# Kernel tuning notes

Hardware: AMD Instinct MI355X
Metric: run time of the kernel (lower is better)

The kernel has to match this reference:

```python
import jax, jax.numpy as jnp
import numpy as np

H = 12        # num_attention_heads
A = 16        # agent_num
C = 768       # hidden_size


def setup_inputs() -> dict:
    key = jax.random.key(0)
    ks = jax.random.split(key, 16)
    B, N = 8, 4096
    std = 0.02
    return {
        "s1_hidden_states": jax.random.normal(ks[0], (B, N, C), jnp.float32),
        "s2_hidden_states": jax.random.normal(ks[1], (B, N, C), jnp.float32),
        "Wq": jax.random.normal(ks[2], (C, C), jnp.float32) * std,
        "bq": jnp.zeros((C,), jnp.float32),
        "Wk": jax.random.normal(ks[3], (C, C), jnp.float32) * std,
        "bk": jnp.zeros((C,), jnp.float32),
        "Wv": jax.random.normal(ks[4], (C, C), jnp.float32) * std,
        "bv": jnp.zeros((C,), jnp.float32),
        "an_bias": jax.random.normal(ks[5], (H, A, 7, 7), jnp.float32) * std,
        "na_bias": jax.random.normal(ks[6], (H, A, 7, 7), jnp.float32) * std,
        "ah_bias": jax.random.normal(ks[7], (1, H, A, A, 1), jnp.float32) * std,
        "aw_bias": jax.random.normal(ks[8], (1, H, A, 1, A), jnp.float32) * std,
        "ha_bias": jax.random.normal(ks[9], (1, H, A, 1, A), jnp.float32) * std,
        "wa_bias": jax.random.normal(ks[10], (1, H, 1, A, A), jnp.float32) * std,
    }


def reference(s1_hidden_states, s2_hidden_states, Wq, bq, Wk, bk, Wv, bv,
              an_bias, na_bias, ah_bias, aw_bias, ha_bias, wa_bias):
    b, n, c = s1_hidden_states.shape
    m = s2_hidden_states.shape[1]
    hd = c // H
    scale = hd ** -0.5

    q = s1_hidden_states @ Wq.T + bq            # (b, n, c)
    k = s2_hidden_states @ Wk.T + bk            # (b, m, c)
    v = s2_hidden_states @ Wv.T + bv            # (b, m, c)

    # AdaptiveAvgPool1d(A) with n % A == 0 -> uniform chunk mean
    agent = q.reshape(b, A, n // A, c).mean(axis=2)  # (b, A, c)

    def heads(x):
        return x.reshape(b, -1, H, hd).transpose(0, 2, 1, 3)

    qh, kh, vh = heads(q), heads(k), heads(v)        # (b,H,·,hd)
    ah = heads(agent)                                # (b,H,A,hd)

    # stage 1: agent -> keys.  bias is constant per (h, a) row.
    pb1 = jax.image.resize(an_bias, (H, A, A, A), method='bilinear').reshape(1, H, A, A * A)
    pb2 = (ah_bias + aw_bias).reshape(1, H, A, A * A)
    pb = (pb1 + pb2).mean(axis=-1)                   # (1, H, A)
    agent_attn = jnp.einsum('bhad,bhmd->bham', ah * scale, kh) + pb[:, :, :, None]
    agent_attn = jax.nn.softmax(agent_attn, axis=-1)
    agent_v = jnp.einsum('bham,bhmd->bhad', agent_attn, vh)  # (b,H,A,hd)

    # stage 2: queries -> agents.
    ab1 = jax.image.resize(na_bias, (H, A, A, A), method='bilinear') \
            .reshape(1, H, A, A * A).transpose(0, 1, 3, 2)   # (1,H,A*A,A)
    ab2 = (ha_bias + wa_bias).reshape(1, H, A * A, A)
    ab = (ab1 + ab2).mean(axis=-2)                   # (1, H, A)
    q_attn = jnp.einsum('bhnd,bhad->bhna', qh * scale, ah) + ab[:, :, None, :]
    q_attn = jax.nn.softmax(q_attn, axis=-1)
    x = jnp.einsum('bhna,bhad->bhnd', q_attn, agent_v)  # (b,H,n,hd)
    return x.transpose(0, 2, 1, 3).reshape(b, n, c)
```

## Files before the change

### kernel.cpp

```cpp
#include <hip/hip_runtime.h>
#include <cstdint>
#include <cstddef>

typedef unsigned short ushort_t;
typedef unsigned int uint;

typedef __attribute__((ext_vector_type(8))) short short8;
typedef __attribute__((ext_vector_type(4))) float floatx4;

#define CDIM 768

__device__ __forceinline__ float bfu(ushort_t u) {
    return __uint_as_float(((uint)u) << 16);
}
__device__ __forceinline__ void bf2(uint u, float& lo, float& hi) {
    lo = __uint_as_float(u << 16);
    hi = __uint_as_float(u & 0xffff0000u);
}
__device__ __forceinline__ ushort_t f2bfu(float f) {
    uint u = __float_as_uint(f);
    u += 0x7fffu + ((u >> 16) & 1u);
    return (ushort_t)(u >> 16);
}
__device__ __forceinline__ uint pack2(float a, float b) {
    return (uint)f2bfu(a) | ((uint)f2bfu(b) << 16);
}
__device__ __forceinline__ uint cvt2(float lo, float hi) {
    uint r;
    asm("v_cvt_pk_bf16_f32 %0, %1, %2" : "=v"(r) : "v"(lo), "v"(hi));
    return r;
}
__device__ __forceinline__ short8 mk8(uint a, uint b, uint c, uint d) {
    union { uint4 u; short8 s; } x;
    x.u = (uint4){a, b, c, d};
    return x.s;
}
__device__ __forceinline__ void gload_lds16(const void* g, void* l) {
    __builtin_amdgcn_global_load_lds(
        (__attribute__((address_space(1))) void*)(uintptr_t)g,
        (__attribute__((address_space(3))) void*)l, 16, 0, 0);
}

__global__ __launch_bounds__(256) void cvt_w(
    const float* __restrict__ Wq, const float* __restrict__ Wk,
    const float* __restrict__ Wv, ushort_t* __restrict__ wb)
{
    const int m = blockIdx.y;
    const float* src = (m == 0) ? Wq : (m == 1 ? Wk : Wv);
    ushort_t* dst = wb + (size_t)m * 589824;
    const int i = (blockIdx.x * 256 + threadIdx.x) * 8;
    const float4 f0 = *(const float4*)(src + i);
    const float4 f1 = *(const float4*)(src + i + 4);
    uint4 u;
    u.x = pack2(f0.x, f0.y);
    u.y = pack2(f0.z, f0.w);
    u.z = pack2(f1.x, f1.y);
    u.w = pack2(f1.z, f1.w);
    *(uint4*)(dst + i) = u;
}

__global__ __launch_bounds__(256) void init_agent(const float* __restrict__ bq,
                                                  float* __restrict__ agent)
{
    const int bh = blockIdx.x;
    const int h = bh % 12;
    for (int i = threadIdx.x; i < 1024; i += 256)
        agent[(size_t)bh * 1024 + i] = bq[h * 64 + (i & 63)];
}

__global__ __launch_bounds__(256, 2) void gemm_qkv(
    const float* __restrict__ s1, const float* __restrict__ s2,
    const ushort_t* __restrict__ wb,
    const float* __restrict__ bq, const float* __restrict__ bk, const float* __restrict__ bv,
    ushort_t* __restrict__ qo, ushort_t* __restrict__ ko, ushort_t* __restrict__ vo,
    float* __restrict__ agent)
{
    const int z = blockIdx.z;
    const float* A        = (z == 0) ? s1 : s2;
    const ushort_t* W     = wb + (size_t)z * 589824;
    const float* bias     = (z == 0) ? bq : (z == 1 ? bk : bv);
    ushort_t* out         = (z == 0) ? qo : (z == 1 ? ko : vo);

    __shared__ ushort_t At[128 * 64];
    __shared__ ushort_t Wt[128 * 64];

    const int tid  = threadIdx.x;
    const int wave = tid >> 6;
    const int lane = tid & 63;
    const int wm = wave >> 1, wn = wave & 1;

    const int id   = blockIdx.x + (blockIdx.y << 8);
    const int id2  = (id & 7) * 192 + (id >> 3);
    const int row0 = (id2 / 6) * 128;
    const int col0 = (id2 % 6) * 128;

    const int sro = lane >> 3;
    const int sch = ((lane & 7) ^ sro) * 8;
    const float*    gaF = A + (size_t)(row0 + wave * 32 + sro) * CDIM + sch;
    const ushort_t* gwB = W + (size_t)(col0 + wave * 32 + sro) * CDIM + sch;

    floatx4 acc[4][4];
    #pragma unroll
    for (int i = 0; i < 4; ++i)
        #pragma unroll
        for (int j = 0; j < 4; ++j)
            acc[i][j] = (floatx4){0.f, 0.f, 0.f, 0.f};

    const int q4 = lane >> 4, r16 = lane & 15;

    float4 ra[4][2];
    #pragma unroll
    for (int i = 0; i < 4; ++i) {
        const float* p = gaF + (size_t)i * 8 * CDIM;
        ra[i][0] = *(const float4*)(p);
        ra[i][1] = *(const float4*)(p + 4);
    }

    for (int kt = 0; kt < CDIM; kt += 64) {
        __syncthreads();
        #pragma unroll
        for (int i = 0; i < 4; ++i)
            gload_lds16(gwB + (size_t)i * 8 * CDIM + kt, &Wt[(wave * 32 + i * 8) * 64]);
        #pragma unroll
        for (int i = 0; i < 4; ++i) {
            uint4 u;
            u.x = cvt2(ra[i][0].x, ra[i][0].y);
            u.y = cvt2(ra[i][0].z, ra[i][0].w);
            u.z = cvt2(ra[i][1].x, ra[i][1].y);
            u.w = cvt2(ra[i][1].z, ra[i][1].w);
            *(uint4*)&At[(wave * 32 + i * 8 + sro) * 64 + (lane & 7) * 8] = u;
        }
        __syncthreads();
        if (kt + 64 < CDIM) {
            #pragma unroll
            for (int i = 0; i < 4; ++i) {
                const float* p = gaF + (size_t)i * 8 * CDIM + kt + 64;
                ra[i][0] = *(const float4*)(p);
                ra[i][1] = *(const float4*)(p + 4);
            }
        }
        #pragma unroll
        for (int ks = 0; ks < 2; ++ks) {
            short8 af[4], bfr[4];
            #pragma unroll
            for (int mt = 0; mt < 4; ++mt) {
                const int row = wm * 64 + mt * 16 + r16;
                const int ch  = (ks * 4 + q4) ^ (row & 7);
                af[mt] = *(const short8*)&At[row * 64 + ch * 8];
            }
            #pragma unroll
            for (int nt = 0; nt < 4; ++nt) {
                const int row = wn * 64 + nt * 16 + r16;
                const int ch  = (ks * 4 + q4) ^ (row & 7);
                bfr[nt] = *(const short8*)&Wt[row * 64 + ch * 8];
            }
            #pragma unroll
            for (int mt = 0; mt < 4; ++mt)
                #pragma unroll
                for (int nt = 0; nt < 4; ++nt)
                    acc[mt][nt] = __builtin_amdgcn_mfma_f32_16x16x32_bf16(
                        af[mt], bfr[nt], acc[mt][nt], 0, 0, 0);
        }
    }

    const int b = row0 >> 12;
    const int m_base = row0 & 4095;
    #pragma unroll
    for (int nt = 0; nt < 4; ++nt) {
        const int col = col0 + wn * 64 + nt * 16 + r16;
        const int h = col >> 6, d = col & 63;
        const float bb = bias[col];
        ushort_t* ob = out + ((size_t)(b * 12 + h) * 4096) * 64 + d;
        float psum = 0.f;
        #pragma unroll
        for (int mt = 0; mt < 4; ++mt) {
            const int m = m_base + wm * 64 + mt * 16 + q4 * 4;
            #pragma unroll
            for (int r = 0; r < 4; ++r) {
                ob[(size_t)(m + r) * 64] = f2bfu(acc[mt][nt][r] + bb);
                psum += acc[mt][nt][r];
            }
        }
        if (z == 0) {
            psum += __shfl_xor(psum, 16);
            psum += __shfl_xor(psum, 32);
            if (q4 == 0)
                atomicAdd(&agent[(size_t)(b * 12 + h) * 1024 + (m_base >> 8) * 64 + d],
                          psum * (1.0f / 256.0f));
        }
    }
}

__global__ void bias_ab_k(const float* __restrict__ na, const float* __restrict__ ha,
                          const float* __restrict__ wa, float* __restrict__ ab)
{
    const int t = threadIdx.x;
    if (t >= 192) return;
    const int h = t >> 4, a = t & 15;
    const float cw[7] = {2.25f, 2.34375f, 2.28125f, 2.25f, 2.28125f, 2.34375f, 2.25f};
    float acc = 0.f;
    const float* nb = na + (h * 16 + a) * 49;
    for (int i = 0; i < 7; ++i)
        for (int j = 0; j < 7; ++j)
            acc += cw[i] * cw[j] * nb[i * 7 + j];
    acc *= (1.0f / 256.0f);
    float s = 0.f;
    for (int p = 0; p < 16; ++p)
        s += ha[(h * 16 + p) * 16 + a] + wa[(h * 16 + p) * 16 + a];
    ab[t] = acc + s * (1.0f / 16.0f);
}

__global__ __launch_bounds__(256) void stage1(
    const ushort_t* __restrict__ k_hm, const ushort_t* __restrict__ v_hm,
    const float* __restrict__ agent, float* __restrict__ Sp, float* __restrict__ avp)
{
    const int bh = blockIdx.x, z = blockIdx.y;
    const int tid = threadIdx.x;
    __shared__ float ahs[1024];
    __shared__ ushort_t E2[512 * 20];

    for (int i = tid; i < 1024; i += 256)
        ahs[i] = agent[(size_t)bh * 1024 + i] * 0.125f;
    __syncthreads();

    const int m0 = z * 512;
    const ushort_t* kb = k_hm + ((size_t)bh * 4096 + m0) * 64;

    {
        const uint4* krA = (const uint4*)(kb + (size_t)tid * 64);
        const uint4* krB = (const uint4*)(kb + (size_t)(tid + 256) * 64);
        uint kuA[16], kuB[16];
        #pragma unroll
        for (int i = 0; i < 4; ++i) {
            uint4 ua = krA[i], ub = krB[i];
            kuA[i*4+0] = ua.x; kuA[i*4+1] = ua.y; kuA[i*4+2] = ua.z; kuA[i*4+3] = ua.w;
            kuB[i*4+0] = ub.x; kuB[i*4+1] = ub.y; kuB[i*4+2] = ub.z; kuB[i*4+3] = ub.w;
        }
        float dsA[16], dsB[16];
        #pragma unroll
        for (int a = 0; a < 16; ++a) { dsA[a] = 0.f; dsB[a] = 0.f; }
        #pragma unroll
        for (int c = 0; c < 16; ++c) {
            float a0, a1, a2, a3, b0, b1, b2, b3;
            bf2(kuA[2*c],   a0, a1); bf2(kuA[2*c+1], a2, a3);
            bf2(kuB[2*c],   b0, b1); bf2(kuB[2*c+1], b2, b3);
            #pragma unroll
            for (int a = 0; a < 16; ++a) {
                const floatx4 av = *(const floatx4*)&ahs[a * 64 + c * 4];
                dsA[a] += a0 * av[0] + a1 * av[1] + a2 * av[2] + a3 * av[3];
                dsB[a] += b0 * av[0] + b1 * av[1] + b2 * av[2] + b3 * av[3];
            }
        }
        uint eA[8], eB[8];
        #pragma unroll
        for (int a2 = 0; a2 < 8; ++a2) {
            eA[a2] = pack2(__expf(dsA[2*a2]), __expf(dsA[2*a2+1]));
            eB[a2] = pack2(__expf(dsB[2*a2]), __expf(dsB[2*a2+1]));
        }
        uint2* dA = (uint2*)&E2[(size_t)tid * 20];
        uint2* dB = (uint2*)&E2[(size_t)(tid + 256) * 20];
        dA[0] = make_uint2(eA[0], eA[1]); dA[1] = make_uint2(eA[2], eA[3]);
        dA[2] = make_uint2(eA[4], eA[5]); dA[3] = make_uint2(eA[6], eA[7]);
        dB[0] = make_uint2(eB[0], eB[1]); dB[1] = make_uint2(eB[2], eB[3]);
        dB[2] = make_uint2(eB[4], eB[5]); dB[3] = make_uint2(eB[6], eB[7]);
    }
    __syncthreads();

    const int d = tid & 63, g = tid >> 6;
    const ushort_t* vb = v_hm + ((size_t)bh * 4096 + m0) * 64 + d;
    float acc0 = 0, acc1 = 0, acc2 = 0, acc3 = 0;
    float ss0 = 0, ss1 = 0, ss2 = 0, ss3 = 0;
    for (int ml = 0; ml < 512; ++ml) {
        const float vv = bfu(vb[(size_t)ml * 64]);
        const uint2 ee = *(const uint2*)&E2[(size_t)ml * 20 + g * 4];
        float e0, e1, e2, e3;
        bf2(ee.x, e0, e1);
        bf2(ee.y, e2, e3);
        acc0 += e0 * vv; ss0 += e0;
        acc1 += e1 * vv; ss1 += e1;
        acc2 += e2 * vv; ss2 += e2;
        acc3 += e3 * vv; ss3 += e3;
    }
    float* avz = avp + (size_t)(z * 96 + bh) * 1024;
    avz[(g * 4 + 0) * 64 + d] = acc0;
    avz[(g * 4 + 1) * 64 + d] = acc1;
    avz[(g * 4 + 2) * 64 + d] = acc2;
    avz[(g * 4 + 3) * 64 + d] = acc3;
    if (d == 0) {
        float* Sz = Sp + (z * 96 + bh) * 16;
        Sz[g * 4 + 0] = ss0;
        Sz[g * 4 + 1] = ss1;
        Sz[g * 4 + 2] = ss2;
        Sz[g * 4 + 3] = ss3;
    }
}

__global__ __launch_bounds__(256) void stage2(
    const ushort_t* __restrict__ q_hm, const float* __restrict__ avp,
    const float* __restrict__ Sp, const float* __restrict__ agent,
    const float* __restrict__ ab, float* __restrict__ out)
{
    const int nb = blockIdx.x;
    const int bh = blockIdx.y;
    const int b = bh / 12, h = bh % 12;
    const int tid = threadIdx.x;
    const int g = (tid >> 4) & 3;
    const int t = tid & 15;
    const int w = tid >> 6;
    __shared__ float avn[1024];

    {
        const int i4 = tid * 4;
        const int a = i4 >> 6;
        floatx4 num = {0.f, 0.f, 0.f, 0.f};
        float den = 0.f;
        #pragma unroll
        for (int zz = 0; zz < 8; ++zz) {
            num += *(const floatx4*)&avp[(size_t)(zz * 96 + bh) * 1024 + i4];
            den += Sp[(zz * 96 + bh) * 16 + a];
        }
        const float r = 1.0f / den;
        *(floatx4*)&avn[i4] = num * r;
    }
    __syncthreads();

    short8 ahA[2], ahE[2];
    #pragma unroll
    for (int k0 = 0; k0 < 2; ++k0) {
        const float* p = agent + (size_t)bh * 1024 + t * 64 + k0 * 32 + g * 8;
        const float4 f0 = *(const float4*)p;
        const float4 f1 = *(const float4*)(p + 4);
        const float v[8] = {f0.x, f0.y, f0.z, f0.w, f1.x, f1.y, f1.z, f1.w};
        uint u[4], e[4];
        #pragma unroll
        for (int j = 0; j < 4; ++j) {
            const float a0 = v[2*j] * 0.125f, a1 = v[2*j+1] * 0.125f;
            u[j] = cvt2(a0, a1);
            float b0, b1; bf2(u[j], b0, b1);
            e[j] = cvt2(a0 - b0, a1 - b1);
        }
        ahA[k0] = mk8(u[0], u[1], u[2], u[3]);
        ahE[k0] = mk8(e[0], e[1], e[2], e[3]);
    }

    short8 avf[4], ave[4];
    #pragma unroll
    for (int dt = 0; dt < 4; ++dt) {
        uint u[4] = {0, 0, 0, 0}, e[4] = {0, 0, 0, 0};
        if (g < 2) {
            #pragma unroll
            for (int j = 0; j < 4; ++j) {
                const float a0 = avn[(8*g + 2*j)     * 64 + dt * 16 + t];
                const float a1 = avn[(8*g + 2*j + 1) * 64 + dt * 16 + t];
                u[j] = cvt2(a0, a1);
                float b0, b1; bf2(u[j], b0, b1);
                e[j] = cvt2(a0 - b0, a1 - b1);
            }
        }
        avf[dt] = mk8(u[0], u[1], u[2], u[3]);
        ave[dt] = mk8(e[0], e[1], e[2], e[3]);
    }

    float abv[4];
    #pragma unroll
    for (int r = 0; r < 4; ++r) abv[r] = ab[h * 16 + 4 * g + r];

    const int src0 = (t + 32 * g) & 63;
    const int src1 = (src0 + 16) & 63;
    const int n0 = nb * 256 + w * 64;
    const ushort_t* qb = q_hm + ((size_t)bh * 4096 + n0) * 64;
    float* ob = out + ((size_t)b * 4096 + n0) * CDIM + h * 64;

    #pragma unroll
    for (int ti = 0; ti < 4; ++ti) {
        const ushort_t* qp = qb + (size_t)(ti * 16 + t) * 64 + g * 8;
        const short8 qB0 = *(const short8*)(qp);
        const short8 qB1 = *(const short8*)(qp + 32);

        floatx4 sc = {0.f, 0.f, 0.f, 0.f};
        sc = __builtin_amdgcn_mfma_f32_16x16x32_bf16(ahA[0], qB0, sc, 0, 0, 0);
        sc = __builtin_amdgcn_mfma_f32_16x16x32_bf16(ahA[1], qB1, sc, 0, 0, 0);
        sc = __builtin_amdgcn_mfma_f32_16x16x32_bf16(ahE[0], qB0, sc, 0, 0, 0);
        sc = __builtin_amdgcn_mfma_f32_16x16x32_bf16(ahE[1], qB1, sc, 0, 0, 0);

        const float e0 = __expf(sc[0] + abv[0]);
        const float e1 = __expf(sc[1] + abv[1]);
        const float e2 = __expf(sc[2] + abv[2]);
        const float e3 = __expf(sc[3] + abv[3]);
        float s = e0 + e1 + e2 + e3;
        s += __shfl_xor(s, 16);
        s += __shfl_xor(s, 32);
        const float rs = 1.0f / s;
        const float p0 = e0 * rs, p1 = e1 * rs, p2 = e2 * rs, p3 = e3 * rs;

        const uint P0 = cvt2(p0, p1), P1 = cvt2(p2, p3);
        float q0, q1, q2, q3;
        bf2(P0, q0, q1); bf2(P1, q2, q3);
        const uint E0 = cvt2(p0 - q0, p1 - q1), E1 = cvt2(p2 - q2, p3 - q3);

        uint w0 = __shfl(P0, src0), w1 = __shfl(P1, src0);
        uint w2 = __shfl(P0, src1), w3 = __shfl(P1, src1);
        uint x0 = __shfl(E0, src0), x1 = __shfl(E1, src0);
        uint x2 = __shfl(E0, src1), x3 = __shfl(E1, src1);
        if (g >= 2) { w0 = w1 = w2 = w3 = 0; x0 = x1 = x2 = x3 = 0; }
        const short8 pf = mk8(w0, w1, w2, w3);
        const short8 pe = mk8(x0, x1, x2, x3);

        float* op = ob + (size_t)(ti * 16 + t) * CDIM + 4 * g;
        #pragma unroll
        for (int dt = 0; dt < 4; ++dt) {
            floatx4 od = {0.f, 0.f, 0.f, 0.f};
            od = __builtin_amdgcn_mfma_f32_16x16x32_bf16(avf[dt], pf, od, 0, 0, 0);
            od = __builtin_amdgcn_mfma_f32_16x16x32_bf16(avf[dt], pe, od, 0, 0, 0);
            od = __builtin_amdgcn_mfma_f32_16x16x32_bf16(ave[dt], pf, od, 0, 0, 0);
            *(floatx4*)(op + dt * 16) = od;
        }
    }
}

extern "C" void kernel_launch(void* const* d_in, const int* in_sizes, int n_in,
                              void* d_out, int out_size, void* d_ws, size_t ws_size,
                              hipStream_t stream) {
    (void)in_sizes; (void)n_in; (void)out_size; (void)ws_size;
    const float* s1 = (const float*)d_in[0];
    const float* s2 = (const float*)d_in[1];
    const float* Wq = (const float*)d_in[2];
    const float* bq = (const float*)d_in[3];
    const float* Wk = (const float*)d_in[4];
    const float* bk = (const float*)d_in[5];
    const float* Wv = (const float*)d_in[6];
    const float* bv = (const float*)d_in[7];
    const float* na = (const float*)d_in[9];
    const float* ha = (const float*)d_in[12];
    const float* wa = (const float*)d_in[13];
    float* out = (float*)d_out;

    char* ws = (char*)d_ws;
    ushort_t* q_hm = (ushort_t*)(ws);
    ushort_t* k_hm = (ushort_t*)(ws + 50331648);
    ushort_t* v_hm = (ushort_t*)(ws + 100663296);
    float* agent   = (float*)(ws + 150994944);
    float* Sp      = (float*)(ws + 151388160);
    float* avp     = (float*)(ws + 151437312);
    float* ab      = (float*)(ws + 154583040);
    ushort_t* wb   = (ushort_t*)(ws + 154583808);

    cvt_w      <<<dim3(288, 3),    256, 0, stream>>>(Wq, Wk, Wv, wb);
    init_agent <<<dim3(96),        256, 0, stream>>>(bq, agent);
    gemm_qkv   <<<dim3(256, 6, 3), 256, 0, stream>>>(s1, s2, wb, bq, bk, bv,
                                                     q_hm, k_hm, v_hm, agent);
    bias_ab_k  <<<1, 256, 0, stream>>>(na, ha, wa, ab);
    stage1     <<<dim3(96, 8),     256, 0, stream>>>(k_hm, v_hm, agent, Sp, avp);
    stage2     <<<dim3(16, 96),    256, 0, stream>>>(q_hm, avp, Sp, agent, ab, out);
}
```

Baseline: 304.4 us.

## Stream fp32 activations directly to LDS and convert to bf16 at fragment load

The A operand of the QKV GEMM was previously loaded into registers one tile ahead, converted to bf16, and written to LDS. It is now copied as fp32 straight into a swizzled LDS tile with direct global-to-LDS loads. The fp32-to-bf16 conversion moves to the point where MFMA fragments are read, and the launch bound is raised to 3 blocks per CU. This frees the prefetch registers and allows more occupancy, at the cost of double the LDS footprint and bandwidth for A. Each fragment is also converted redundantly by every wave that reads it, and the register-level prefetch overlap is lost.

After: 309.4 us. About the same (+1.6%).

```diff
diff --git a/kernel.cpp b/kernel.cpp
--- a/kernel.cpp
+++ b/kernel.cpp
@@ -68,7 +68,7 @@
         agent[(size_t)bh * 1024 + i] = bq[h * 64 + (i & 63)];
 }
 
-__global__ __launch_bounds__(256, 2) void gemm_qkv(
+__global__ __launch_bounds__(256, 3) void gemm_qkv(
     const float* __restrict__ s1, const float* __restrict__ s2,
     const ushort_t* __restrict__ wb,
     const float* __restrict__ bq, const float* __restrict__ bk, const float* __restrict__ bv,
@@ -81,7 +81,7 @@
     const float* bias     = (z == 0) ? bq : (z == 1 ? bk : bv);
     ushort_t* out         = (z == 0) ? qo : (z == 1 ? ko : vo);
 
-    __shared__ ushort_t At[128 * 64];
+    __shared__ float    At[128 * 64];
     __shared__ ushort_t Wt[128 * 64];
 
     const int tid  = threadIdx.x;
@@ -94,10 +94,13 @@
     const int row0 = (id2 / 6) * 128;
     const int col0 = (id2 % 6) * 128;
 
-    const int sro = lane >> 3;
-    const int sch = ((lane & 7) ^ sro) * 8;
-    const float*    gaF = A + (size_t)(row0 + wave * 32 + sro) * CDIM + sch;
-    const ushort_t* gwB = W + (size_t)(col0 + wave * 32 + sro) * CDIM + sch;
+    const int sroW = lane >> 3;
+    const int schW = ((lane & 7) ^ sroW) * 8;
+    const ushort_t* gwB = W + (size_t)(col0 + wave * 32 + sroW) * CDIM + schW;
+
+    const int rlA = lane >> 4;
+    const int pcr = (lane & 15) ^ rlA;
+    const float* gaRow = A + (size_t)(row0 + wave * 32 + rlA) * CDIM;
 
     floatx4 acc[4][4];
     #pragma unroll
@@ -108,45 +111,29 @@
 
     const int q4 = lane >> 4, r16 = lane & 15;
 
-    float4 ra[4][2];
-    #pragma unroll
-    for (int i = 0; i < 4; ++i) {
-        const float* p = gaF + (size_t)i * 8 * CDIM;
-        ra[i][0] = *(const float4*)(p);
-        ra[i][1] = *(const float4*)(p + 4);
-    }
-
     for (int kt = 0; kt < CDIM; kt += 64) {
         __syncthreads();
         #pragma unroll
         for (int i = 0; i < 4; ++i)
             gload_lds16(gwB + (size_t)i * 8 * CDIM + kt, &Wt[(wave * 32 + i * 8) * 64]);
         #pragma unroll
-        for (int i = 0; i < 4; ++i) {
-            uint4 u;
-            u.x = cvt2(ra[i][0].x, ra[i][0].y);
-            u.y = cvt2(ra[i][0].z, ra[i][0].w);
-            u.z = cvt2(ra[i][1].x, ra[i][1].y);
-            u.w = cvt2(ra[i][1].z, ra[i][1].w);
-            *(uint4*)&At[(wave * 32 + i * 8 + sro) * 64 + (lane & 7) * 8] = u;
+        for (int i = 0; i < 8; ++i) {
+            const int c4 = pcr ^ ((4 * i) & 15);
+            gload_lds16(gaRow + (size_t)(i * 4) * CDIM + kt + c4 * 4,
+                        &At[(wave * 32 + i * 4) * 64]);
         }
         __syncthreads();
-        if (kt + 64 < CDIM) {
-            #pragma unroll
-            for (int i = 0; i < 4; ++i) {
-                const float* p = gaF + (size_t)i * 8 * CDIM + kt + 64;
-                ra[i][0] = *(const float4*)(p);
-                ra[i][1] = *(const float4*)(p + 4);
-            }
-        }
         #pragma unroll
         for (int ks = 0; ks < 2; ++ks) {
             short8 af[4], bfr[4];
             #pragma unroll
             for (int mt = 0; mt < 4; ++mt) {
                 const int row = wm * 64 + mt * 16 + r16;
-                const int ch  = (ks * 4 + q4) ^ (row & 7);
-                af[mt] = *(const short8*)&At[row * 64 + ch * 8];
+                const int c0  = (ks * 8 + q4 * 2) ^ r16;
+                const floatx4 fa = *(const floatx4*)&At[row * 64 + c0 * 4];
+                const floatx4 fb = *(const floatx4*)&At[row * 64 + (c0 ^ 1) * 4];
+                af[mt] = mk8(cvt2(fa[0], fa[1]), cvt2(fa[2], fa[3]),
+                             cvt2(fb[0], fb[1]), cvt2(fb[2], fb[3]));
             }
             #pragma unroll
             for (int nt = 0; nt < 4; ++nt) {
```

## Pre-convert activations to bf16 and double stage1 threads per block

Applied to the files above, without the earlier changes.

Adds a separate kernel that converts s1/s2 to bf16 in workspace so the QKV GEMM can load A tiles with direct global-to-LDS loads instead of fp32 register loads plus conversion. Stage1 now runs 512 threads per block, each handling one key row, and splits the value reduction into two halves, which doubles the partial buffers that stage2 reduces. The conversion adds an extra full read and write of both activation tensors (about 200MB of traffic) in exchange for a simpler, better-pipelined GEMM loop. avp now aliases the activation buffer, which is safe only because gemm finishes before stage1.

Result: slower. 312.5 us (+2.6%).

```diff
diff --git a/kernel.cpp b/kernel.cpp
--- a/kernel.cpp
+++ b/kernel.cpp
@@ -59,6 +59,24 @@
     *(uint4*)(dst + i) = u;
 }
 
+__global__ __launch_bounds__(256) void cvt_a(
+    const float* __restrict__ s1, const float* __restrict__ s2,
+    ushort_t* __restrict__ ab)
+{
+    const int m = blockIdx.y;
+    const float* src = (m == 0) ? s1 : s2;
+    ushort_t* dst = ab + (size_t)m * 25165824;
+    const size_t i = ((size_t)blockIdx.x * 256 + threadIdx.x) * 8;
+    const float4 f0 = *(const float4*)(src + i);
+    const float4 f1 = *(const float4*)(src + i + 4);
+    uint4 u;
+    u.x = pack2(f0.x, f0.y);
+    u.y = pack2(f0.z, f0.w);
+    u.z = pack2(f1.x, f1.y);
+    u.w = pack2(f1.z, f1.w);
+    *(uint4*)(dst + i) = u;
+}
+
 __global__ __launch_bounds__(256) void init_agent(const float* __restrict__ bq,
                                                   float* __restrict__ agent)
 {
@@ -69,14 +87,13 @@
 }
 
 __global__ __launch_bounds__(256, 2) void gemm_qkv(
-    const float* __restrict__ s1, const float* __restrict__ s2,
-    const ushort_t* __restrict__ wb,
+    const ushort_t* __restrict__ ab, const ushort_t* __restrict__ wb,
     const float* __restrict__ bq, const float* __restrict__ bk, const float* __restrict__ bv,
     ushort_t* __restrict__ qo, ushort_t* __restrict__ ko, ushort_t* __restrict__ vo,
     float* __restrict__ agent)
 {
     const int z = blockIdx.z;
-    const float* A        = (z == 0) ? s1 : s2;
+    const ushort_t* A     = ab + (size_t)(z != 0) * 25165824;
     const ushort_t* W     = wb + (size_t)z * 589824;
     const float* bias     = (z == 0) ? bq : (z == 1 ? bk : bv);
     ushort_t* out         = (z == 0) ? qo : (z == 1 ? ko : vo);
@@ -96,8 +113,8 @@
 
     const int sro = lane >> 3;
     const int sch = ((lane & 7) ^ sro) * 8;
-    const float*    gaF = A + (size_t)(row0 + wave * 32 + sro) * CDIM + sch;
-    const ushort_t* gwB = W + (size_t)(col0 + wave * 32 + sro) * CDIM + sch;
+    const ushort_t* gaBase = A + (size_t)(row0 + wave * 32 + sro) * CDIM + sch;
+    const ushort_t* gwBase = W + (size_t)(col0 + wave * 32 + sro) * CDIM + sch;
 
     floatx4 acc[4][4];
     #pragma unroll
@@ -108,37 +125,14 @@
 
     const int q4 = lane >> 4, r16 = lane & 15;
 
-    float4 ra[4][2];
-    #pragma unroll
-    for (int i = 0; i < 4; ++i) {
-        const float* p = gaF + (size_t)i * 8 * CDIM;
-        ra[i][0] = *(const float4*)(p);
-        ra[i][1] = *(const float4*)(p + 4);
-    }
-
     for (int kt = 0; kt < CDIM; kt += 64) {
         __syncthreads();
         #pragma unroll
-        for (int i = 0; i < 4; ++i)
-            gload_lds16(gwB + (size_t)i * 8 * CDIM + kt, &Wt[(wave * 32 + i * 8) * 64]);
-        #pragma unroll
         for (int i = 0; i < 4; ++i) {
-            uint4 u;
-            u.x = cvt2(ra[i][0].x, ra[i][0].y);
-            u.y = cvt2(ra[i][0].z, ra[i][0].w);
-            u.z = cvt2(ra[i][1].x, ra[i][1].y);
-            u.w = cvt2(ra[i][1].z, ra[i][1].w);
-            *(uint4*)&At[(wave * 32 + i * 8 + sro) * 64 + (lane & 7) * 8] = u;
+            gload_lds16(gaBase + (size_t)i * 8 * CDIM + kt, &At[(wave * 32 + i * 8) * 64]);
+            gload_lds16(gwBase + (size_t)i * 8 * CDIM + kt, &Wt[(wave * 32 + i * 8) * 64]);
         }
         __syncthreads();
-        if (kt + 64 < CDIM) {
-            #pragma unroll
-            for (int i = 0; i < 4; ++i) {
-                const float* p = gaF + (size_t)i * 8 * CDIM + kt + 64;
-                ra[i][0] = *(const float4*)(p);
-                ra[i][1] = *(const float4*)(p + 4);
-            }
-        }
         #pragma unroll
         for (int ks = 0; ks < 2; ++ks) {
             short8 af[4], bfr[4];
@@ -210,7 +204,7 @@
     ab[t] = acc + s * (1.0f / 16.0f);
 }
 
-__global__ __launch_bounds__(256) void stage1(
+__global__ __launch_bounds__(512) void stage1(
     const ushort_t* __restrict__ k_hm, const ushort_t* __restrict__ v_hm,
     const float* __restrict__ agent, float* __restrict__ Sp, float* __restrict__ avp)
 {
@@ -219,7 +213,7 @@
     __shared__ float ahs[1024];
     __shared__ ushort_t E2[512 * 20];
 
-    for (int i = tid; i < 1024; i += 256)
+    for (int i = tid; i < 1024; i += 512)
         ahs[i] = agent[(size_t)bh * 1024 + i] * 0.125f;
     __syncthreads();
 
@@ -227,52 +221,44 @@
     const ushort_t* kb = k_hm + ((size_t)bh * 4096 + m0) * 64;
 
     {
-        const uint4* krA = (const uint4*)(kb + (size_t)tid * 64);
-        const uint4* krB = (const uint4*)(kb + (size_t)(tid + 256) * 64);
-        uint kuA[16], kuB[16];
+        const uint4* kr = (const uint4*)(kb + (size_t)tid * 64);
+        uint ku[16];
         #pragma unroll
         for (int i = 0; i < 4; ++i) {
-            uint4 ua = krA[i], ub = krB[i];
-            kuA[i*4+0] = ua.x; kuA[i*4+1] = ua.y; kuA[i*4+2] = ua.z; kuA[i*4+3] = ua.w;
-            kuB[i*4+0] = ub.x; kuB[i*4+1] = ub.y; kuB[i*4+2] = ub.z; kuB[i*4+3] = ub.w;
-        }
-        float dsA[16], dsB[16];
-        #pragma unroll
-        for (int a = 0; a < 16; ++a) { dsA[a] = 0.f; dsB[a] = 0.f; }
+            uint4 ua = kr[i];
+            ku[i*4+0] = ua.x; ku[i*4+1] = ua.y; ku[i*4+2] = ua.z; ku[i*4+3] = ua.w;
+        }
+        float ds[16];
+        #pragma unroll
+        for (int a = 0; a < 16; ++a) ds[a] = 0.f;
         #pragma unroll
         for (int c = 0; c < 16; ++c) {
-            float a0, a1, a2, a3, b0, b1, b2, b3;
-            bf2(kuA[2*c],   a0, a1); bf2(kuA[2*c+1], a2, a3);
-            bf2(kuB[2*c],   b0, b1); bf2(kuB[2*c+1], b2, b3);
+            float a0, a1, a2, a3;
+            bf2(ku[2*c],   a0, a1); bf2(ku[2*c+1], a2, a3);
             #pragma unroll
             for (int a = 0; a < 16; ++a) {
                 const floatx4 av = *(const floatx4*)&ahs[a * 64 + c * 4];
-                dsA[a] += a0 * av[0] + a1 * av[1] + a2 * av[2] + a3 * av[3];
-                dsB[a] += b0 * av[0] + b1 * av[1] + b2 * av[2] + b3 * av[3];
+                ds[a] += a0 * av[0] + a1 * av[1] + a2 * av[2] + a3 * av[3];
             }
         }
-        uint eA[8], eB[8];
-        #pragma unroll
-        for (int a2 = 0; a2 < 8; ++a2) {
-            eA[a2] = pack2(__expf(dsA[2*a2]), __expf(dsA[2*a2+1]));
-            eB[a2] = pack2(__expf(dsB[2*a2]), __expf(dsB[2*a2+1]));
-        }
+        uint e[8];
+        #pragma unroll
+        for (int a2 = 0; a2 < 8; ++a2)
+            e[a2] = pack2(__expf(ds[2*a2]), __expf(ds[2*a2+1]));
         uint2* dA = (uint2*)&E2[(size_t)tid * 20];
-        uint2* dB = (uint2*)&E2[(size_t)(tid + 256) * 20];
-        dA[0] = make_uint2(eA[0], eA[1]); dA[1] = make_uint2(eA[2], eA[3]);
-        dA[2] = make_uint2(eA[4], eA[5]); dA[3] = make_uint2(eA[6], eA[7]);
-        dB[0] = make_uint2(eB[0], eB[1]); dB[1] = make_uint2(eB[2], eB[3]);
-        dB[2] = make_uint2(eB[4], eB[5]); dB[3] = make_uint2(eB[6], eB[7]);
+        dA[0] = make_uint2(e[0], e[1]); dA[1] = make_uint2(e[2], e[3]);
+        dA[2] = make_uint2(e[4], e[5]); dA[3] = make_uint2(e[6], e[7]);
     }
     __syncthreads();
 
-    const int d = tid & 63, g = tid >> 6;
-    const ushort_t* vb = v_hm + ((size_t)bh * 4096 + m0) * 64 + d;
+    const int d = tid & 63, g = (tid >> 6) & 3, half = tid >> 8;
+    const int mb = half * 256;
+    const ushort_t* vb = v_hm + ((size_t)bh * 4096 + m0 + mb) * 64 + d;
     float acc0 = 0, acc1 = 0, acc2 = 0, acc3 = 0;
     float ss0 = 0, ss1 = 0, ss2 = 0, ss3 = 0;
-    for (int ml = 0; ml < 512; ++ml) {
+    for (int ml = 0; ml < 256; ++ml) {
         const float vv = bfu(vb[(size_t)ml * 64]);
-        const uint2 ee = *(const uint2*)&E2[(size_t)ml * 20 + g * 4];
+        const uint2 ee = *(const uint2*)&E2[(size_t)(mb + ml) * 20 + g * 4];
         float e0, e1, e2, e3;
         bf2(ee.x, e0, e1);
         bf2(ee.y, e2, e3);
@@ -281,13 +267,14 @@
         acc2 += e2 * vv; ss2 += e2;
         acc3 += e3 * vv; ss3 += e3;
     }
-    float* avz = avp + (size_t)(z * 96 + bh) * 1024;
+    const int z2 = z * 2 + half;
+    float* avz = avp + (size_t)(z2 * 96 + bh) * 1024;
     avz[(g * 4 + 0) * 64 + d] = acc0;
     avz[(g * 4 + 1) * 64 + d] = acc1;
     avz[(g * 4 + 2) * 64 + d] = acc2;
     avz[(g * 4 + 3) * 64 + d] = acc3;
     if (d == 0) {
-        float* Sz = Sp + (z * 96 + bh) * 16;
+        float* Sz = Sp + (z2 * 96 + bh) * 16;
         Sz[g * 4 + 0] = ss0;
         Sz[g * 4 + 1] = ss1;
         Sz[g * 4 + 2] = ss2;
@@ -315,7 +302,7 @@
         floatx4 num = {0.f, 0.f, 0.f, 0.f};
         float den = 0.f;
         #pragma unroll
-        for (int zz = 0; zz < 8; ++zz) {
+        for (int zz = 0; zz < 16; ++zz) {
             num += *(const floatx4*)&avp[(size_t)(zz * 96 + bh) * 1024 + i4];
             den += Sp[(zz * 96 + bh) * 16 + a];
         }
@@ -441,15 +428,17 @@
     ushort_t* v_hm = (ushort_t*)(ws + 100663296);
     float* agent   = (float*)(ws + 150994944);
     float* Sp      = (float*)(ws + 151388160);
-    float* avp     = (float*)(ws + 151437312);
-    float* ab      = (float*)(ws + 154583040);
-    ushort_t* wb   = (ushort_t*)(ws + 154583808);
+    float* ab      = (float*)(ws + 151486464);
+    ushort_t* wb   = (ushort_t*)(ws + 151487232);
+    ushort_t* abuf = (ushort_t*)(ws + 155026176);
+    float* avp     = (float*)(ws + 155026176);
 
     cvt_w      <<<dim3(288, 3),    256, 0, stream>>>(Wq, Wk, Wv, wb);
+    cvt_a      <<<dim3(12288, 2),  256, 0, stream>>>(s1, s2, abuf);
     init_agent <<<dim3(96),        256, 0, stream>>>(bq, agent);
-    gemm_qkv   <<<dim3(256, 6, 3), 256, 0, stream>>>(s1, s2, wb, bq, bk, bv,
+    gemm_qkv   <<<dim3(256, 6, 3), 256, 0, stream>>>(abuf, wb, bq, bk, bv,
                                                      q_hm, k_hm, v_hm, agent);
     bias_ab_k  <<<1, 256, 0, stream>>>(na, ha, wa, ab);
-    stage1     <<<dim3(96, 8),     256, 0, stream>>>(k_hm, v_hm, agent, Sp, avp);
+    stage1     <<<dim3(96, 8),     512, 0, stream>>>(k_hm, v_hm, agent, Sp, avp);
     stage2     <<<dim3(16, 96),    256, 0, stream>>>(q_hm, avp, Sp, agent, ab, out);
 }
```
